# Optimization experiments

Hardware: AMD Instinct MI355X
Metric: run time of the kernel (lower is better)

The kernel has to match this reference:

```python
import jax, jax.numpy as jnp
import numpy as np

ATOM, BOND, INNER, HID, REC, OHID = 14, 3, 20, 34, 20, 25
N_NODES = 1048576
N_EDGES = 983040
MAX_DEPTH = 16
N_GRAPHS = 16384


def leaky(x):
    return jnp.where(x >= 0, x, 0.01 * x)


def setup_inputs() -> dict:
    key = jax.random.key(0)
    ks = jax.random.split(key, 20)
    p = 0.02
    atom_feats = jax.random.normal(ks[0], (N_NODES, ATOM), jnp.float32)
    bond_feats = jax.random.normal(ks[1], (N_EDGES, BOND), jnp.float32)
    # build a forest: node i's parent is some node with strictly smaller depth.
    # For a jit-friendly synthetic instance we assign depths and connect each
    # non-root node (edge) from a parent at depth d to child at depth d+1.
    depth = np.asarray(jax.random.randint(ks[2], (N_NODES,), 0, MAX_DEPTH))
    order = np.argsort(depth, kind='stable')
    depth_sorted = depth[order]
    # edges: child must have depth >= 1; pick children among nodes with depth>0
    child_pool = order[depth_sorted > 0]
    rng = np.random.default_rng(0)
    child_idx = rng.choice(child_pool, size=N_EDGES, replace=False) if len(child_pool) >= N_EDGES else rng.choice(child_pool, size=N_EDGES, replace=True)
    child_depth = depth[child_idx]
    # parent: random node with depth == child_depth - 1
    # bucket nodes by depth
    buckets = [order[depth_sorted == d] for d in range(MAX_DEPTH)]
    parent_idx = np.empty(N_EDGES, dtype=np.int64)
    for d in range(1, MAX_DEPTH):
        m = child_depth == d
        if m.sum() > 0:
            parent_idx[m] = rng.choice(buckets[d - 1], size=int(m.sum()))
    graph_id = np.asarray(jax.random.randint(ks[3], (N_NODES,), 0, N_GRAPHS))
    # roots: nodes with no incoming edge (not a child)
    is_child = np.zeros(N_NODES, dtype=bool)
    is_child[child_idx] = True
    is_root = (~is_child).astype(np.float32)
    params = {
        'inner_w': jax.random.normal(ks[4], (REC + BOND, INNER), jnp.float32) * p,
        'inner_b': jnp.zeros((INNER,), jnp.float32),
        'net_w1': jax.random.normal(ks[5], (INNER + ATOM, HID), jnp.float32) * p,
        'net_b1': jnp.zeros((HID,), jnp.float32),
        'net_w2': jax.random.normal(ks[6], (HID, REC), jnp.float32) * p,
        'net_b2': jnp.zeros((REC,), jnp.float32),
        'net0_w1': jax.random.normal(ks[7], (ATOM, HID), jnp.float32) * p,
        'net0_b1': jnp.zeros((HID,), jnp.float32),
        'net0_w2': jax.random.normal(ks[8], (HID, REC), jnp.float32) * p,
        'net0_b2': jnp.zeros((REC,), jnp.float32),
        'out_w1': jax.random.normal(ks[9], (REC, OHID), jnp.float32) * p,
        'out_b1': jnp.zeros((OHID,), jnp.float32),
        'out_w2': jax.random.normal(ks[10], (OHID, 1), jnp.float32) * p,
        'out_b2': jnp.zeros((1,), jnp.float32),
    }
    return dict(atom_feats=atom_feats, bond_feats=bond_feats,
                parent_idx=jnp.asarray(parent_idx), child_idx=jnp.asarray(child_idx),
                node_depth=jnp.asarray(depth), graph_id=jnp.asarray(graph_id),
                is_root=jnp.asarray(is_root), **params)


def reference(atom_feats, bond_feats, parent_idx, child_idx, node_depth, graph_id,
              is_root, inner_w, inner_b, net_w1, net_b1, net_w2, net_b2,
              net0_w1, net0_b1, net0_w2, net0_b2, out_w1, out_b1, out_w2, out_b2):
    n_nodes = atom_feats.shape[0]
    has_child = jnp.zeros((n_nodes,), jnp.float32).at[parent_idx].add(1.0) > 0
    # leaf vector via net0
    leaf_vec = leaky(leaky(atom_feats @ net0_w1 + net0_b1) @ net0_w2 + net0_b2)  # [N, REC]
    h = leaf_vec  # node recursive vectors; internal nodes filled bottom-up
    # process depths from deepest-1 parents up to 0: at step d, update nodes at depth d
    for d in range(MAX_DEPTH - 2, -1, -1):
        child_h = h[child_idx]  # [E, REC]
        msg = leaky(jnp.concatenate([bond_feats, child_h], axis=1) @ inner_w + inner_b)  # [E, INNER]
        # only edges whose parent is at depth d contribute this step
        edge_mask = (node_depth[parent_idx] == d).astype(msg.dtype)[:, None]
        inner_sum = jnp.zeros((n_nodes, INNER), msg.dtype).at[parent_idx].add(msg * edge_mask)
        x = jnp.concatenate([atom_feats, inner_sum], axis=1)  # [N, ATOM+INNER]
        new_h = leaky(leaky(x @ net_w1 + net_b1) @ net_w2 + net_b2)
        upd = ((node_depth == d) & has_child).astype(h.dtype)[:, None]
        h = h * (1.0 - upd) + new_h * upd
    # sum root vectors per graph
    root_h = h * is_root[:, None]
    g = jax.ops.segment_sum(root_h, graph_id, num_segments=N_GRAPHS)  # [G, REC]
    out = jnp.tanh(g @ out_w1 + out_b1) @ out_w2 + out_b2  # [G, 1]
    return out.reshape(-1)
```

## Files before the change

### kernel.cpp

```cpp
#include <hip/hip_runtime.h>

#define ATOM  14
#define BOND  3
#define INNER 20
#define HID   34
#define HIDP  36
#define REC   20
#define OHID  25
#define NN    1048576
#define NE    983040
#define NG    16384

#define NB    512
#define NT    256
#define GT    (NB*NT)
#define SPAN  (NN/NB)
#define SE    (SPAN/NT)

#define NB2   1024
#define NT2   256
#define NGRP  (NT2/4)
#define SSTR  (NGRP+1)
#define NBINS (NB2*32)

__device__ __forceinline__ float leaky(float x) { return x >= 0.f ? x : 0.01f * x; }

__device__ __forceinline__ void wsync() {
    __builtin_amdgcn_wave_barrier();
    __builtin_amdgcn_sched_barrier(0);
}

__device__ __forceinline__ void gbar_f(int* bar, int goal) {
    __syncthreads();
    if (threadIdx.x == 0) {
        __threadfence();
        __hip_atomic_fetch_add(bar, 1, __ATOMIC_RELEASE, __HIP_MEMORY_SCOPE_AGENT);
        while (__hip_atomic_load(bar, __ATOMIC_RELAXED, __HIP_MEMORY_SCOPE_AGENT) < goal)
            __builtin_amdgcn_s_sleep(32);
        __threadfence();
    }
    __syncthreads();
}

__global__ void k_pre(int* cnt_n, int* pnode, float* g, int* bin_cnt, int* totals, int* bars) {
    int tid = blockIdx.x * 256 + threadIdx.x;
    for (int i = tid; i < NN; i += 262144) { cnt_n[i] = 0; pnode[i] = i; }
    for (int i = tid; i < NG * REC; i += 262144) g[i] = 0.f;
    for (int i = tid; i < NBINS; i += 262144) bin_cnt[i] = 0;
    if (tid == 0) { totals[0] = 0; totals[16] = 0; }
    if (tid == 1) for (int k = 0; k < 32; ++k) bars[k] = 0;
}

__global__ __launch_bounds__(NT) void k_prep(
    const int* __restrict__ parent, const int* __restrict__ child,
    const int* __restrict__ depth, const int* __restrict__ gid,
    const float* __restrict__ isr, const float* __restrict__ bond,
    int* cnt_n, int* pnode, int* r1, int* r2,
    int* K_s, int* cnt_s, int* row_ptr, int* adjc, float4* bond_s4,
    int* bin_cnt, int* bin_base, int* bin_cur,
    int* totals, int* bar)
{
    __shared__ int sh[NT];
    __shared__ int sbase_sh;
    const int t = threadIdx.x;
    const int tid = blockIdx.x * NT + t;
    int ep = 0;

    for (int e = tid; e < NE; e += GT) {
        atomicAdd(&cnt_n[parent[e]], 1);
        pnode[child[e]] = parent[e];
    }
    gbar_f(bar, NB * ++ep);

    for (int i = tid; i < NN; i += GT) {
        int d = depth[i];
        int r = i;
        for (int s = 0; s < d; ++s) r = pnode[r];
        int K = (r & (NB2 - 1)) * 32 + d * 2 + (cnt_n[i] == 0 ? 1 : 0);
        K_s[i] = K;
        atomicAdd(&bin_cnt[K], 1);
    }
    gbar_f(bar, NB * ++ep);

    if (blockIdx.x < NBINS / NT) {
        int k0 = blockIdx.x * NT + t;
        int v = bin_cnt[k0];
        sh[t] = v;
        __syncthreads();
        for (int ofs = 1; ofs < NT; ofs <<= 1) {
            int x = (t >= ofs) ? sh[t - ofs] : 0;
            __syncthreads();
            sh[t] += x;
            __syncthreads();
        }
        if (t == NT - 1) sbase_sh = atomicAdd(&totals[0], sh[t]);
        __syncthreads();
        int b = sbase_sh + sh[t] - v;
        bin_base[k0] = b;
        bin_cur[k0] = b;
    }
    gbar_f(bar, NB * ++ep);

    for (int i = tid; i < NN; i += GT) {
        int pos = atomicAdd(&bin_cur[K_s[i]], 1);
        pnode[pos] = i;
        r1[i] = pos;
        r2[pos] = (isr[i] != 0.f) ? gid[i] : -1;
        cnt_s[pos] = cnt_n[i];
    }
    gbar_f(bar, NB * ++ep);

    {
        int base0 = blockIdx.x * SPAN + t * SE;
        int v[SE]; int sum = 0;
        #pragma unroll
        for (int k = 0; k < SE; ++k) { v[k] = cnt_s[base0 + k]; sum += v[k]; }
        __syncthreads();
        sh[t] = sum;
        __syncthreads();
        for (int ofs = 1; ofs < NT; ofs <<= 1) {
            int x = (t >= ofs) ? sh[t - ofs] : 0;
            __syncthreads();
            sh[t] += x;
            __syncthreads();
        }
        if (t == NT - 1) sbase_sh = atomicAdd(&totals[16], sh[t]);
        __syncthreads();
        int run = sbase_sh + sh[t] - sum;
        #pragma unroll
        for (int k = 0; k < SE; ++k) { row_ptr[base0 + k] = run; cnt_n[base0 + k] = run; run += v[k]; }
    }
    gbar_f(bar, NB * ++ep);

    for (int e = tid; e < NE; e += GT) {
        int cpos = r1[child[e]];
        int pp   = r1[parent[e]];
        int slot = atomicAdd(&cnt_n[pp], 1);
        adjc[slot] = cpos;
        bond_s4[cpos] = make_float4(bond[(size_t)e * BOND], bond[(size_t)e * BOND + 1],
                                    bond[(size_t)e * BOND + 2], 0.f);
    }
}

__device__ __forceinline__ void coop_mlp(int slot, int j, int KN,
                                         const float* xs, float* hs, float* os,
                                         const float* w1, const float* b1,
                                         const float* w2, const float* b2,
                                         float* o)
{
    wsync();
    float acc[9];
    #pragma unroll
    for (int u = 0; u < 9; ++u) { int h = 9*j + u; acc[u] = (h < HID) ? b1[h] : 0.f; }
    #pragma unroll 2
    for (int k = 0; k < KN; ++k) {
        float xk = xs[k * SSTR + slot];
        #pragma unroll
        for (int u = 0; u < 9; ++u) { int h = 9*j + u; if (h < HID) acc[u] += xk * w1[k * HIDP + h]; }
    }
    #pragma unroll
    for (int u = 0; u < 9; ++u) { int h = 9*j + u; if (h < HID) hs[h * SSTR + slot] = leaky(acc[u]); }
    wsync();
    #pragma unroll
    for (int u = 0; u < 5; ++u) o[u] = b2[5*j + u];
    #pragma unroll 2
    for (int k = 0; k < HID; ++k) {
        float hk = hs[k * SSTR + slot];
        #pragma unroll
        for (int u = 0; u < 5; ++u) o[u] += hk * w2[k * REC + 5*j + u];
    }
    #pragma unroll
    for (int u = 0; u < 5; ++u) { o[u] = leaky(o[u]); os[(5*j + u) * SSTR + slot] = o[u]; }
    wsync();
}

__global__ __launch_bounds__(NT2) void k_levels(
    const float* __restrict__ atom,
    const int* __restrict__ node_list, const int* __restrict__ groot_s,
    const int* __restrict__ cnt_s, const int* __restrict__ row_ptr,
    const int* __restrict__ adjc, const float4* __restrict__ bond_s4,
    const int* __restrict__ bin_base, const int* __restrict__ bin_cnt,
    const float* __restrict__ iw, const float* __restrict__ ib,
    const float* __restrict__ nw1, const float* __restrict__ nb1,
    const float* __restrict__ nw2, const float* __restrict__ nb2,
    const float* __restrict__ l0w1, const float* __restrict__ l0b1,
    const float* __restrict__ l0w2, const float* __restrict__ l0b2,
    float* __restrict__ g, float* __restrict__ msg_s)
{
    __shared__ float lw1[34 * HIDP];
    __shared__ float lw2[HID * REC];
    __shared__ float liw[23 * REC];
    __shared__ float zw1[ATOM * HIDP];
    __shared__ float zw2[HID * REC];
    __shared__ float lb1[HID], lb2[REC], lbi[INNER], zb1[HID], zb2[REC];
    __shared__ float xs[34 * SSTR];
    __shared__ float hs[34 * SSTR];
    __shared__ float os[20 * SSTR];

    const int t = threadIdx.x;
    const int b = blockIdx.x;
    const int slot = t >> 2;
    const int j = t & 3;

    for (int idx = t; idx < 34 * HIDP; idx += NT2) {
        int r = idx / HIDP, c = idx - r * HIDP;
        lw1[idx] = (c < HID) ? nw1[r * HID + c] : 0.f;
    }
    for (int idx = t; idx < HID * REC; idx += NT2) { lw2[idx] = nw2[idx]; zw2[idx] = l0w2[idx]; }
    for (int idx = t; idx < 23 * REC; idx += NT2) liw[idx] = iw[idx];
    for (int idx = t; idx < ATOM * HIDP; idx += NT2) {
        int r = idx / HIDP, c = idx - r * HIDP;
        zw1[idx] = (c < HID) ? l0w1[r * HID + c] : 0.f;
    }
    if (t < HID) { lb1[t] = nb1[t]; zb1[t] = l0b1[t]; }
    else if (t >= 64 && t < 64 + REC) { lb2[t - 64] = nb2[t - 64]; zb2[t - 64] = l0b2[t - 64]; }
    if (t >= 96 && t < 96 + INNER) lbi[t - 96] = ib[t - 96];
    __syncthreads();

    for (int d = 15; d >= 0; --d) {
        {
            int K = b * 32 + d * 2;
            int base = bin_base[K], n0 = bin_cnt[K];
            for (int idx = slot; idx < n0; idx += NGRP) {
                int pos = base + idx;
                int n   = cnt_s[pos];
                int i   = node_list[pos];
                int gr  = groot_s[pos];
                int rp0 = row_ptr[pos];
                float s0 = 0.f, s1 = 0.f, s2 = 0.f, s3 = 0.f, s4 = 0.f;
                for (int r = rp0; r < rp0 + n; ++r) {
                    const float* mp = msg_s + (size_t)adjc[r] * REC + 5*j;
                    s0 += mp[0]; s1 += mp[1]; s2 += mp[2]; s3 += mp[3]; s4 += mp[4];
                }
                const float* ar = atom + (size_t)i * ATOM;
                #pragma unroll
                for (int u = 0; u < 4; ++u) { int k = 4*j + u; if (k < ATOM) xs[k * SSTR + slot] = ar[k]; }
                xs[(ATOM + 5*j + 0) * SSTR + slot] = s0;
                xs[(ATOM + 5*j + 1) * SSTR + slot] = s1;
                xs[(ATOM + 5*j + 2) * SSTR + slot] = s2;
                xs[(ATOM + 5*j + 3) * SSTR + slot] = s3;
                xs[(ATOM + 5*j + 4) * SSTR + slot] = s4;
                float o[5];
                coop_mlp(slot, j, ATOM + INNER, xs, hs, os, lw1, lb1, lw2, lb2, o);
                if (gr >= 0) {
                    #pragma unroll
                    for (int u = 0; u < 5; ++u) atomicAdd(&g[(size_t)gr * REC + 5*j + u], o[u]);
                } else {
                    float4 b4 = bond_s4[pos];
                    float m[5];
                    #pragma unroll
                    for (int u = 0; u < 5; ++u)
                        m[u] = lbi[5*j + u] + b4.x * liw[0 * INNER + 5*j + u]
                             + b4.y * liw[1 * INNER + 5*j + u] + b4.z * liw[2 * INNER + 5*j + u];
                    #pragma unroll 2
                    for (int k = 0; k < REC; ++k) {
                        float ok = os[k * SSTR + slot];
                        #pragma unroll
                        for (int u = 0; u < 5; ++u) m[u] += ok * liw[(BOND + k) * INNER + 5*j + u];
                    }
                    #pragma unroll
                    for (int u = 0; u < 5; ++u) msg_s[(size_t)pos * REC + 5*j + u] = leaky(m[u]);
                }
            }
        }
        {
            int K = b * 32 + d * 2 + 1;
            int base = bin_base[K], n1 = bin_cnt[K];
            for (int idx = slot; idx < n1; idx += NGRP) {
                int pos = base + idx;
                int i  = node_list[pos];
                int gr = groot_s[pos];
                const float* ar = atom + (size_t)i * ATOM;
                #pragma unroll
                for (int u = 0; u < 4; ++u) { int k = 4*j + u; if (k < ATOM) xs[k * SSTR + slot] = ar[k]; }
                float o[5];
                coop_mlp(slot, j, ATOM, xs, hs, os, zw1, zb1, zw2, zb2, o);
                if (gr >= 0) {
                    #pragma unroll
                    for (int u = 0; u < 5; ++u) atomicAdd(&g[(size_t)gr * REC + 5*j + u], o[u]);
                } else {
                    float4 b4 = bond_s4[pos];
                    float m[5];
                    #pragma unroll
                    for (int u = 0; u < 5; ++u)
                        m[u] = lbi[5*j + u] + b4.x * liw[0 * INNER + 5*j + u]
                             + b4.y * liw[1 * INNER + 5*j + u] + b4.z * liw[2 * INNER + 5*j + u];
                    #pragma unroll 2
                    for (int k = 0; k < REC; ++k) {
                        float ok = os[k * SSTR + slot];
                        #pragma unroll
                        for (int u = 0; u < 5; ++u) m[u] += ok * liw[(BOND + k) * INNER + 5*j + u];
                    }
                    #pragma unroll
                    for (int u = 0; u < 5; ++u) msg_s[(size_t)pos * REC + 5*j + u] = leaky(m[u]);
                }
            }
        }
        __threadfence_block();
        __syncthreads();
    }
}

__global__ void k_out(const float* __restrict__ g,
                      const float* __restrict__ w1, const float* __restrict__ b1,
                      const float* __restrict__ w2, const float* __restrict__ b2,
                      float* __restrict__ out) {
    int t = blockIdx.x * 256 + threadIdx.x;
    if (t >= NG) return;
    const float* gv = g + (size_t)t * REC;
    float gl[REC];
    #pragma unroll
    for (int k = 0; k < REC; ++k) gl[k] = gv[k];
    float acc = b2[0];
    for (int j = 0; j < OHID; ++j) {
        float s = b1[j];
        #pragma unroll
        for (int k = 0; k < REC; ++k) s += gl[k] * w1[k * OHID + j];
        acc += tanhf(s) * w2[j];
    }
    out[t] = acc;
}

extern "C" void kernel_launch(void* const* d_in, const int* in_sizes, int n_in,
                              void* d_out, int out_size, void* d_ws, size_t ws_size,
                              hipStream_t stream) {
    const float* atom    = (const float*)d_in[0];
    const float* bond    = (const float*)d_in[1];
    const int*   parent  = (const int*)d_in[2];
    const int*   child   = (const int*)d_in[3];
    const int*   depth   = (const int*)d_in[4];
    const int*   gid     = (const int*)d_in[5];
    const float* isr     = (const float*)d_in[6];
    const float* inner_w = (const float*)d_in[7];
    const float* inner_b = (const float*)d_in[8];
    const float* net_w1  = (const float*)d_in[9];
    const float* net_b1  = (const float*)d_in[10];
    const float* net_w2  = (const float*)d_in[11];
    const float* net_b2  = (const float*)d_in[12];
    const float* net0_w1 = (const float*)d_in[13];
    const float* net0_b1 = (const float*)d_in[14];
    const float* net0_w2 = (const float*)d_in[15];
    const float* net0_b2 = (const float*)d_in[16];
    const float* out_w1  = (const float*)d_in[17];
    const float* out_b1  = (const float*)d_in[18];
    const float* out_w2  = (const float*)d_in[19];
    const float* out_b2  = (const float*)d_in[20];
    float* out = (float*)d_out;

    char* ws = (char*)d_ws;
    size_t o = 0;
    float* msg_s    = (float*)(ws + o);  o += (size_t)NN * REC * 4;
    float4* bond_s4 = (float4*)(ws + o); o += (size_t)NN * 16;
    float* g        = (float*)(ws + o);  o += (size_t)NG * REC * 4;
    int* adjc       = (int*)(ws + o);    o += (size_t)NE * 4;
    int* cnt_n      = (int*)(ws + o);    o += (size_t)NN * 4;
    int* pnode      = (int*)(ws + o);    o += (size_t)NN * 4;
    int* r1         = (int*)(ws + o);    o += (size_t)NN * 4;
    int* r2         = (int*)(ws + o);    o += (size_t)NN * 4;
    int* K_s        = (int*)(ws + o);    o += (size_t)NN * 4;
    int* cnt_s      = (int*)(ws + o);    o += (size_t)NN * 4;
    int* row_ptr    = (int*)(ws + o);    o += (size_t)NN * 4;
    int* bin_cnt    = (int*)(ws + o);    o += (size_t)NBINS * 4;
    int* bin_base   = (int*)(ws + o);    o += (size_t)NBINS * 4;
    int* bin_cur    = (int*)(ws + o);    o += (size_t)NBINS * 4;
    int* totals     = (int*)(ws + o);    o += 32 * 4;
    int* bars       = (int*)(ws + o);    o += 32 * 4;

    k_pre<<<1024, 256, 0, stream>>>(cnt_n, pnode, g, bin_cnt, totals, bars);
    k_prep<<<NB, NT, 0, stream>>>(parent, child, depth, gid, isr, bond,
                                  cnt_n, pnode, r1, r2, K_s, cnt_s, row_ptr,
                                  adjc, bond_s4, bin_cnt, bin_base, bin_cur,
                                  totals, bars);
    k_levels<<<NB2, NT2, 0, stream>>>(atom, pnode , r2 ,
                                      cnt_s, row_ptr, adjc, bond_s4,
                                      bin_base, bin_cnt,
                                      inner_w, inner_b, net_w1, net_b1, net_w2, net_b2,
                                      net0_w1, net0_b1, net0_w2, net0_b2,
                                      g, msg_s);
    k_out<<<(NG + 255) / 256, 256, 0, stream>>>(g, out_w1, out_b1, out_w2, out_b2, out);
}
```

Before: 956.7 us.

## Pack per-node metadata into int4 and read bond features by edge id

Per-node sorted metadata (node id, child count, root graph id, incoming edge id) is packed into one int4 array, and the parent pointer is stored together with the incoming edge id. This removes the separate node_list, groot_s and cnt_s arrays and the permuted float4 bond copy. The final prep pass now loops over sorted nodes instead of edges when building the adjacency list. The level kernel gathers bond features directly from the original bond array using the stored edge id. That trades a scatter pass in prep for uncoalesced 3-float gathers during the levels.

```diff
diff --git a/kernel.cpp b/kernel.cpp
--- a/kernel.cpp
+++ b/kernel.cpp
@@ -42,9 +42,9 @@
     __syncthreads();
 }
 
-__global__ void k_pre(int* cnt_n, int* pnode, float* g, int* bin_cnt, int* totals, int* bars) {
+__global__ void k_pre(int* cnt_n, int2* pnode2, float* g, int* bin_cnt, int* totals, int* bars) {
     int tid = blockIdx.x * 256 + threadIdx.x;
-    for (int i = tid; i < NN; i += 262144) { cnt_n[i] = 0; pnode[i] = i; }
+    for (int i = tid; i < NN; i += 262144) { cnt_n[i] = 0; pnode2[i] = make_int2(i, -1); }
     for (int i = tid; i < NG * REC; i += 262144) g[i] = 0.f;
     for (int i = tid; i < NBINS; i += 262144) bin_cnt[i] = 0;
     if (tid == 0) { totals[0] = 0; totals[16] = 0; }
@@ -54,9 +54,9 @@
 __global__ __launch_bounds__(NT) void k_prep(
     const int* __restrict__ parent, const int* __restrict__ child,
     const int* __restrict__ depth, const int* __restrict__ gid,
-    const float* __restrict__ isr, const float* __restrict__ bond,
-    int* cnt_n, int* pnode, int* r1, int* r2,
-    int* K_s, int* cnt_s, int* row_ptr, int* adjc, float4* bond_s4,
+    const float* __restrict__ isr,
+    int* cnt_n, int2* pnode2, int* inv, int* K_s,
+    int4* nodeinfo, int* row_ptr, int* adjc,
     int* bin_cnt, int* bin_base, int* bin_cur,
     int* totals, int* bar)
 {
@@ -68,14 +68,14 @@
 
     for (int e = tid; e < NE; e += GT) {
         atomicAdd(&cnt_n[parent[e]], 1);
-        pnode[child[e]] = parent[e];
+        pnode2[child[e]] = make_int2(parent[e], e);
     }
     gbar_f(bar, NB * ++ep);
 
     for (int i = tid; i < NN; i += GT) {
         int d = depth[i];
         int r = i;
-        for (int s = 0; s < d; ++s) r = pnode[r];
+        for (int s = 0; s < d; ++s) r = pnode2[r].x;
         int K = (r & (NB2 - 1)) * 32 + d * 2 + (cnt_n[i] == 0 ? 1 : 0);
         K_s[i] = K;
         atomicAdd(&bin_cnt[K], 1);
@@ -103,10 +103,10 @@
 
     for (int i = tid; i < NN; i += GT) {
         int pos = atomicAdd(&bin_cur[K_s[i]], 1);
-        pnode[pos] = i;
-        r1[i] = pos;
-        r2[pos] = (isr[i] != 0.f) ? gid[i] : -1;
-        cnt_s[pos] = cnt_n[i];
+        int2 pe = pnode2[i];
+        int gr = (isr[i] != 0.f) ? gid[i] : -1;
+        nodeinfo[pos] = make_int4(i, cnt_n[i], gr, pe.y);
+        inv[i] = pos;
     }
     gbar_f(bar, NB * ++ep);
 
@@ -114,7 +114,7 @@
         int base0 = blockIdx.x * SPAN + t * SE;
         int v[SE]; int sum = 0;
         #pragma unroll
-        for (int k = 0; k < SE; ++k) { v[k] = cnt_s[base0 + k]; sum += v[k]; }
+        for (int k = 0; k < SE; ++k) { v[k] = nodeinfo[base0 + k].y; sum += v[k]; }
         __syncthreads();
         sh[t] = sum;
         __syncthreads();
@@ -132,13 +132,14 @@
     }
     gbar_f(bar, NB * ++ep);
 
-    for (int e = tid; e < NE; e += GT) {
-        int cpos = r1[child[e]];
-        int pp   = r1[parent[e]];
-        int slot = atomicAdd(&cnt_n[pp], 1);
-        adjc[slot] = cpos;
-        bond_s4[cpos] = make_float4(bond[(size_t)e * BOND], bond[(size_t)e * BOND + 1],
-                                    bond[(size_t)e * BOND + 2], 0.f);
+    for (int pos = tid; pos < NN; pos += GT) {
+        int4 ni = nodeinfo[pos];
+        if (ni.w >= 0) {
+            int ppn = pnode2[ni.x].x;
+            int pp  = inv[ppn];
+            int slot = atomicAdd(&cnt_n[pp], 1);
+            adjc[slot] = pos;
+        }
     }
 }
 
@@ -175,10 +176,9 @@
 }
 
 __global__ __launch_bounds__(NT2) void k_levels(
-    const float* __restrict__ atom,
-    const int* __restrict__ node_list, const int* __restrict__ groot_s,
-    const int* __restrict__ cnt_s, const int* __restrict__ row_ptr,
-    const int* __restrict__ adjc, const float4* __restrict__ bond_s4,
+    const float* __restrict__ atom, const float* __restrict__ bond,
+    const int4* __restrict__ nodeinfo, const int* __restrict__ row_ptr,
+    const int* __restrict__ adjc,
     const int* __restrict__ bin_base, const int* __restrict__ bin_cnt,
     const float* __restrict__ iw, const float* __restrict__ ib,
     const float* __restrict__ nw1, const float* __restrict__ nb1,
@@ -223,16 +223,14 @@
             int base = bin_base[K], n0 = bin_cnt[K];
             for (int idx = slot; idx < n0; idx += NGRP) {
                 int pos = base + idx;
-                int n   = cnt_s[pos];
-                int i   = node_list[pos];
-                int gr  = groot_s[pos];
+                int4 ni = nodeinfo[pos];
                 int rp0 = row_ptr[pos];
                 float s0 = 0.f, s1 = 0.f, s2 = 0.f, s3 = 0.f, s4 = 0.f;
-                for (int r = rp0; r < rp0 + n; ++r) {
+                for (int r = rp0; r < rp0 + ni.y; ++r) {
                     const float* mp = msg_s + (size_t)adjc[r] * REC + 5*j;
                     s0 += mp[0]; s1 += mp[1]; s2 += mp[2]; s3 += mp[3]; s4 += mp[4];
                 }
-                const float* ar = atom + (size_t)i * ATOM;
+                const float* ar = atom + (size_t)ni.x * ATOM;
                 #pragma unroll
                 for (int u = 0; u < 4; ++u) { int k = 4*j + u; if (k < ATOM) xs[k * SSTR + slot] = ar[k]; }
                 xs[(ATOM + 5*j + 0) * SSTR + slot] = s0;
@@ -242,16 +240,17 @@
                 xs[(ATOM + 5*j + 4) * SSTR + slot] = s4;
                 float o[5];
                 coop_mlp(slot, j, ATOM + INNER, xs, hs, os, lw1, lb1, lw2, lb2, o);
-                if (gr >= 0) {
-                    #pragma unroll
-                    for (int u = 0; u < 5; ++u) atomicAdd(&g[(size_t)gr * REC + 5*j + u], o[u]);
+                if (ni.z >= 0) {
+                    #pragma unroll
+                    for (int u = 0; u < 5; ++u) atomicAdd(&g[(size_t)ni.z * REC + 5*j + u], o[u]);
                 } else {
-                    float4 b4 = bond_s4[pos];
+                    const float* br = bond + (size_t)ni.w * BOND;
+                    float b0 = br[0], b1 = br[1], b2 = br[2];
                     float m[5];
                     #pragma unroll
                     for (int u = 0; u < 5; ++u)
-                        m[u] = lbi[5*j + u] + b4.x * liw[0 * INNER + 5*j + u]
-                             + b4.y * liw[1 * INNER + 5*j + u] + b4.z * liw[2 * INNER + 5*j + u];
+                        m[u] = lbi[5*j + u] + b0 * liw[0 * INNER + 5*j + u]
+                             + b1 * liw[1 * INNER + 5*j + u] + b2 * liw[2 * INNER + 5*j + u];
                     #pragma unroll 2
                     for (int k = 0; k < REC; ++k) {
                         float ok = os[k * SSTR + slot];
@@ -268,23 +267,23 @@
             int base = bin_base[K], n1 = bin_cnt[K];
             for (int idx = slot; idx < n1; idx += NGRP) {
                 int pos = base + idx;
-                int i  = node_list[pos];
-                int gr = groot_s[pos];
-                const float* ar = atom + (size_t)i * ATOM;
+                int4 ni = nodeinfo[pos];
+                const float* ar = atom + (size_t)ni.x * ATOM;
                 #pragma unroll
                 for (int u = 0; u < 4; ++u) { int k = 4*j + u; if (k < ATOM) xs[k * SSTR + slot] = ar[k]; }
                 float o[5];
                 coop_mlp(slot, j, ATOM, xs, hs, os, zw1, zb1, zw2, zb2, o);
-                if (gr >= 0) {
-                    #pragma unroll
-                    for (int u = 0; u < 5; ++u) atomicAdd(&g[(size_t)gr * REC + 5*j + u], o[u]);
+                if (ni.z >= 0) {
+                    #pragma unroll
+                    for (int u = 0; u < 5; ++u) atomicAdd(&g[(size_t)ni.z * REC + 5*j + u], o[u]);
                 } else {
-                    float4 b4 = bond_s4[pos];
+                    const float* br = bond + (size_t)ni.w * BOND;
+                    float b0 = br[0], b1 = br[1], b2 = br[2];
                     float m[5];
                     #pragma unroll
                     for (int u = 0; u < 5; ++u)
-                        m[u] = lbi[5*j + u] + b4.x * liw[0 * INNER + 5*j + u]
-                             + b4.y * liw[1 * INNER + 5*j + u] + b4.z * liw[2 * INNER + 5*j + u];
+                        m[u] = lbi[5*j + u] + b0 * liw[0 * INNER + 5*j + u]
+                             + b1 * liw[1 * INNER + 5*j + u] + b2 * liw[2 * INNER + 5*j + u];
                     #pragma unroll 2
                     for (int k = 0; k < REC; ++k) {
                         float ok = os[k * SSTR + slot];
@@ -350,15 +349,13 @@
     char* ws = (char*)d_ws;
     size_t o = 0;
     float* msg_s    = (float*)(ws + o);  o += (size_t)NN * REC * 4;
-    float4* bond_s4 = (float4*)(ws + o); o += (size_t)NN * 16;
+    int4* nodeinfo  = (int4*)(ws + o);   o += (size_t)NN * 16;
     float* g        = (float*)(ws + o);  o += (size_t)NG * REC * 4;
+    int2* pnode2    = (int2*)(ws + o);   o += (size_t)NN * 8;
     int* adjc       = (int*)(ws + o);    o += (size_t)NE * 4;
     int* cnt_n      = (int*)(ws + o);    o += (size_t)NN * 4;
-    int* pnode      = (int*)(ws + o);    o += (size_t)NN * 4;
-    int* r1         = (int*)(ws + o);    o += (size_t)NN * 4;
-    int* r2         = (int*)(ws + o);    o += (size_t)NN * 4;
+    int* inv        = (int*)(ws + o);    o += (size_t)NN * 4;
     int* K_s        = (int*)(ws + o);    o += (size_t)NN * 4;
-    int* cnt_s      = (int*)(ws + o);    o += (size_t)NN * 4;
     int* row_ptr    = (int*)(ws + o);    o += (size_t)NN * 4;
     int* bin_cnt    = (int*)(ws + o);    o += (size_t)NBINS * 4;
     int* bin_base   = (int*)(ws + o);    o += (size_t)NBINS * 4;
@@ -366,13 +363,11 @@
     int* totals     = (int*)(ws + o);    o += 32 * 4;
     int* bars       = (int*)(ws + o);    o += 32 * 4;
 
-    k_pre<<<1024, 256, 0, stream>>>(cnt_n, pnode, g, bin_cnt, totals, bars);
-    k_prep<<<NB, NT, 0, stream>>>(parent, child, depth, gid, isr, bond,
-                                  cnt_n, pnode, r1, r2, K_s, cnt_s, row_ptr,
-                                  adjc, bond_s4, bin_cnt, bin_base, bin_cur,
-                                  totals, bars);
-    k_levels<<<NB2, NT2, 0, stream>>>(atom, pnode , r2 ,
-                                      cnt_s, row_ptr, adjc, bond_s4,
+    k_pre<<<1024, 256, 0, stream>>>(cnt_n, pnode2, g, bin_cnt, totals, bars);
+    k_prep<<<NB, NT, 0, stream>>>(parent, child, depth, gid, isr,
+                                  cnt_n, pnode2, inv, K_s, nodeinfo, row_ptr,
+                                  adjc, bin_cnt, bin_base, bin_cur, totals, bars);
+    k_levels<<<NB2, NT2, 0, stream>>>(atom, bond, nodeinfo, row_ptr, adjc,
                                       bin_base, bin_cnt,
                                       inner_w, inner_b, net_w1, net_b1, net_w2, net_b2,
                                       net0_w1, net0_b1, net0_w2, net0_b2,
```

After: 951.7 us. No clear change (-0.5%).
